# Kernel tuning notes

Measured on AMD Instinct MI355X. Metric: run time of the kernel, lower is better.

## Reference

```python
import jax, jax.numpy as jnp
import numpy as np

THETA = 10000.0
H, D_NOPE, D_ROPE, D_V = 12, 64, 64, 128
D_MODEL, D_LAT = 768, 128
B, S = 4, 2048


def _rope(x, pos, theta=THETA):
    # x: (B, S, D) with D even; pos: (S,) int. Matches RoPE.forward exactly
    # (interleaved even/odd rotation, freqs over full flattened D).
    D = x.shape[-1]
    inv_freq = 1.0 / theta ** (jnp.arange(0, D, 2, dtype=jnp.float32) / D)
    ang = pos.astype(jnp.float32)[:, None] * inv_freq        # (S, D/2)
    c, s = jnp.cos(ang), jnp.sin(ang)
    xe, xo = x[..., 0::2], x[..., 1::2]
    out = jnp.stack([xe * c - xo * s, xe * s + xo * c], axis=-1)
    return out.reshape(x.shape)


def setup_inputs() -> dict:
    key = jax.random.key(0)
    ks = jax.random.split(key, 12)
    std = 0.02
    inp = {
        'x': jax.random.normal(ks[0], (B, S, D_MODEL), jnp.float32),
        'token_positions': jnp.arange(S, dtype=jnp.int64) if jax.config.jax_enable_x64 else jnp.arange(S, dtype=jnp.int32),
        'W_dkv': jax.random.normal(ks[1], (D_LAT, D_MODEL), jnp.float32) * std,
        'b_dkv': jnp.zeros((D_LAT,), jnp.float32),
        'W_dq': jax.random.normal(ks[2], (D_LAT, D_MODEL), jnp.float32) * std,
        'b_dq': jnp.zeros((D_LAT,), jnp.float32),
        'W_uk_nope': jax.random.normal(ks[3], (H * D_NOPE, D_LAT), jnp.float32) * std,
        'b_uk_nope': jnp.zeros((H * D_NOPE,), jnp.float32),
        'W_uv': jax.random.normal(ks[4], (H * D_V, D_LAT), jnp.float32) * std,
        'b_uv': jnp.zeros((H * D_V,), jnp.float32),
        'W_uq_nope': jax.random.normal(ks[5], (H * D_NOPE, D_LAT), jnp.float32) * std,
        'b_uq_nope': jnp.zeros((H * D_NOPE,), jnp.float32),
        'W_uq_rope': jax.random.normal(ks[6], (H * D_ROPE, D_LAT), jnp.float32) * std,
        'b_uq_rope': jnp.zeros((H * D_ROPE,), jnp.float32),
        'W_uk_rope': jax.random.normal(ks[7], (H * D_ROPE, D_MODEL), jnp.float32) * std,
        'b_uk_rope': jnp.zeros((H * D_ROPE,), jnp.float32),
        'W_o': jax.random.normal(ks[8], (D_MODEL, H * D_V), jnp.float32) * std,
        'b_o': jnp.zeros((D_MODEL,), jnp.float32),
    }
    return inp


def reference(x, token_positions, W_dkv, b_dkv, W_dq, b_dq,
              W_uk_nope, b_uk_nope, W_uv, b_uv, W_uq_nope, b_uq_nope,
              W_uq_rope, b_uq_rope, W_uk_rope, b_uk_rope, W_o, b_o):
    b, s, _ = x.shape
    lin = lambda t, W, bb: t @ W.T + bb
    d_qk = D_NOPE + D_ROPE  # 128

    C_kv = lin(x, W_dkv, b_dkv)               # (B,S,128)
    C_q = lin(x, W_dq, b_dq)                  # (B,S,128)

    q_nope = lin(C_q, W_uq_nope, b_uq_nope)   # (B,S,H*64)
    k_nope = lin(C_kv, W_uk_nope, b_uk_nope)  # (B,S,H*64)
    v = lin(C_kv, W_uv, b_uv)                 # (B,S,H*128)

    q_rope = _rope(lin(C_q, W_uq_rope, b_uq_rope), token_positions)
    k_rope = _rope(lin(x, W_uk_rope, b_uk_rope), token_positions)

    # Faithful to torch: concat flattened nope||rope then view into heads.
    q = jnp.concatenate([q_nope, q_rope], axis=-1).reshape(b, s, H, d_qk).transpose(0, 2, 1, 3)
    k = jnp.concatenate([k_nope, k_rope], axis=-1).reshape(b, s, H, d_qk).transpose(0, 2, 1, 3)
    vh = v.reshape(b, s, H, D_V).transpose(0, 2, 1, 3)

    scale = 1.0 / jnp.sqrt(jnp.asarray(d_qk, x.dtype))
    logits = jnp.einsum('bhqd,bhkd->bhqk', q, k) * scale
    causal = jnp.tril(jnp.ones((s, s), bool))
    logits = jnp.where(causal, logits, jnp.finfo(logits.dtype).min)
    attn = jax.nn.softmax(logits, axis=-1)
    o = jnp.einsum('bhqk,bhkd->bhqd', attn, vh)      # (B,H,S,Dv)
    o = o.transpose(0, 2, 1, 3).reshape(b, s, H * D_V)
    return o @ W_o.T + b_o
```

## Files before the change

### kernel.cpp

```cpp
#include <hip/hip_runtime.h>

typedef __attribute__((ext_vector_type(8))) short short8;
typedef __attribute__((ext_vector_type(4))) short short4v;
typedef __attribute__((ext_vector_type(2))) int int2v;
typedef __attribute__((ext_vector_type(4))) float float4v;

#define MFMA16(a, b, c) __builtin_amdgcn_mfma_f32_16x16x32_bf16((a), (b), (c), 0, 0, 0)

__device__ __forceinline__ short f2bf(float f) {
  unsigned u = __float_as_uint(f);
  u += 0x7fffu + ((u >> 16) & 1u);
  return (short)(u >> 16);
}

__device__ __forceinline__ int cvtpk(float a, float b) {
  int r;
  asm("v_cvt_pk_bf16_f32 %0, %1, %2" : "=v"(r) : "v"(a), "v"(b));
  return r;
}

__device__ __forceinline__ void glds16(const short* g, short* l) {
  __builtin_amdgcn_global_load_lds(
      (const __attribute__((address_space(1))) void*)g,
      (__attribute__((address_space(3))) void*)l, 16, 0, 0);
}

struct CastSeg { const float* src; short* dst; int n4; };
struct CastArgs { CastSeg seg[9]; int start[10]; };

__global__ __launch_bounds__(256) void castk(CastArgs a) {
  int blk = blockIdx.x;
  int si = 0;
#pragma unroll
  for (int i = 1; i < 9; i++) si += (blk >= a.start[i]);
  int i = (blk - a.start[si]) * 256 + threadIdx.x;
  if (i >= a.seg[si].n4) return;
  float4v f = ((const float4v*)a.seg[si].src)[i];
  short4v o;
  o[0] = f2bf(f[0]); o[1] = f2bf(f[1]); o[2] = f2bf(f[2]); o[3] = f2bf(f[3]);
  ((short4v*)a.seg[si].dst)[i] = o;
}

struct GSeg {
  const short* A;
  const short* W;
  const float* bias0;
  const float* bias1;
  void* outp;
  int lda, ldw, bsplit, ropestart, ldo, ocol, K, flags;
};
struct GArgs { GSeg s[3]; int start[4]; };

__device__ __forceinline__ void gemm_body(const GArgs& ga, const int* __restrict__ pos) {
  int by = blockIdx.y;
  int si = (by >= ga.start[1]) + (by >= ga.start[2]);
  const GSeg sg = ga.s[si];
  int tid = threadIdx.x, w = tid >> 6, lane = tid & 63;
  int quad = lane >> 4, l16 = lane & 15;
  bool ropeF = sg.flags & 1, scaleF = sg.flags & 2;
  bool vtF = sg.flags & 4, f32F = sg.flags & 8, pairF = sg.flags & 16;
  int bm = blockIdx.x * 128;
  int bn = (by - ga.start[si]) * (pairF ? 256 : 128);
  int wm = (w & 1) * 64, wn = (w >> 1) * 64;
  int lda = sg.lda, ldw = sg.ldw;

  __shared__ short At[2][128 * 64];
  __shared__ short Bt[2][128 * 64];

  int srow[4], soff[4];
#pragma unroll
  for (int j = 0; j < 4; j++) {
    int r = w * 32 + j * 8 + (lane >> 3);
    srow[j] = r;
    soff[j] = ((lane & 7) ^ (r & 7)) << 3;
  }
  const short* Ag = sg.A + (size_t)bm * lda;
  const short* Wg = sg.W + (size_t)bn * ldw;

  float4v acc[4][4];
  float4v z = {0.f, 0.f, 0.f, 0.f};
#pragma unroll
  for (int mi = 0; mi < 4; mi++)
#pragma unroll
    for (int ni = 0; ni < 4; ni++) acc[mi][ni] = z;

  auto comp = [&](const short* Ab, const short* Bb) {
#pragma unroll
    for (int ks = 0; ks < 2; ks++) {
      short8 af[4], bf[4];
#pragma unroll
      for (int mi = 0; mi < 4; mi++) {
        int row = wm + mi * 16 + l16;
        af[mi] = *(const short8*)&Ab[(row << 6) + ((((ks << 2) + quad) ^ (row & 7)) << 3)];
      }
#pragma unroll
      for (int ni = 0; ni < 4; ni++) {
        int row = wn + ni * 16 + l16;
        bf[ni] = *(const short8*)&Bb[(row << 6) + ((((ks << 2) + quad) ^ (row & 7)) << 3)];
      }
#pragma unroll
      for (int mi = 0; mi < 4; mi++)
#pragma unroll
        for (int ni = 0; ni < 4; ni++)
          acc[mi][ni] = MFMA16(af[mi], bf[ni], acc[mi][ni]);
    }
  };

  auto epi = [&](int bnX) {
    if (vtF) {
      __syncthreads();
      short* T = &At[0][0];
#pragma unroll
      for (int ni = 0; ni < 4; ni++) {
        int col = wn + ni * 16 + l16;
        float bv = sg.bias0[bnX + col];
#pragma unroll
        for (int mi = 0; mi < 4; mi++) {
          int row0 = wm + mi * 16 + quad * 4;
          int rr = (row0 + ((col & 15) << 3)) & 127;
          short4v ov;
#pragma unroll
          for (int r = 0; r < 4; r++) ov[r] = f2bf(acc[mi][ni][r] + bv);
          *(short4v*)&T[col * 128 + rr] = ov;
        }
      }
      __syncthreads();
      int bidx = bm >> 11, s0 = bm & 2047;
      int sc = tid & 15;
#pragma unroll
      for (int cc = 0; cc < 8; cc++) {
        int c = cc * 16 + (tid >> 4);
        int rr = ((sc + (c & 15)) << 3) & 127;
        short8 v = *(const short8*)&T[c * 128 + rr];
        *(short8*)((short*)sg.outp + ((size_t)(bidx * 1536 + bnX + c)) * 2048 +
                   s0 + (sc << 3)) = v;
      }
      return;
    }
#pragma unroll
    for (int ni = 0; ni < 4; ni++) {
      int col = bnX + wn + ni * 16 + l16;
      float bv = (col < sg.bsplit) ? sg.bias0[col] : sg.bias1[col - sg.bsplit];
      float fr = 0.f;
      bool dorope = ropeF && (col >= sg.ropestart);
      if (dorope) {
        int ri = (col - sg.ropestart) & ~1;
        fr = exp2f((float)ri * (-13.287712379549449f / 768.0f));
      }
#pragma unroll
      for (int mi = 0; mi < 4; mi++) {
        int row0 = bm + wm + mi * 16 + quad * 4;
#pragma unroll
        for (int r = 0; r < 4; r++) {
          int row = row0 + r;
          float v = acc[mi][ni][r] + bv;
          if (ropeF) {
            float pv = __shfl_xor(v, 1, 64);
            if (dorope) {
              float ang = (float)pos[row & 2047] * fr;
              float sn, cs;
              __sincosf(ang, &sn, &cs);
              v = (col & 1) ? (pv * sn + v * cs) : (v * cs - pv * sn);
            }
          }
          if (scaleF) v *= 0.12751743f;
          if (f32F)
            ((float*)sg.outp)[(size_t)row * sg.ldo + sg.ocol + col] = v;
          else
            ((short*)sg.outp)[(size_t)row * sg.ldo + sg.ocol + col] = f2bf(v);
        }
      }
    }
  };

  int nk = sg.K >> 6;
  if (nk == 2) {
    auto stageB = [&](const short* Wg2) {
#pragma unroll
      for (int j = 0; j < 4; j++) {
        glds16(Wg2 + (size_t)srow[j] * ldw + soff[j], &Bt[0][(w * 32 + j * 8) * 64]);
        glds16(Wg2 + (size_t)srow[j] * ldw + 64 + soff[j], &Bt[1][(w * 32 + j * 8) * 64]);
      }
    };
#pragma unroll
    for (int j = 0; j < 4; j++) {
      glds16(Ag + (size_t)srow[j] * lda + soff[j], &At[0][(w * 32 + j * 8) * 64]);
      glds16(Ag + (size_t)srow[j] * lda + 64 + soff[j], &At[1][(w * 32 + j * 8) * 64]);
    }
    stageB(Wg);
    __syncthreads();
    comp(At[0], Bt[0]);
    comp(At[1], Bt[1]);
    if (pairF) {
      __syncthreads();
      stageB(Wg + (size_t)128 * ldw);
      epi(bn);
#pragma unroll
      for (int mi = 0; mi < 4; mi++)
#pragma unroll
        for (int ni = 0; ni < 4; ni++) acc[mi][ni] = z;
      __syncthreads();
      comp(At[0], Bt[0]);
      comp(At[1], Bt[1]);
      epi(bn + 128);
    } else {
      epi(bn);
    }
  } else {
#pragma unroll
    for (int j = 0; j < 4; j++)
      glds16(Ag + (size_t)srow[j] * lda + soff[j], &At[0][(w * 32 + j * 8) * 64]);
#pragma unroll
    for (int j = 0; j < 4; j++)
      glds16(Wg + (size_t)srow[j] * ldw + soff[j], &Bt[0][(w * 32 + j * 8) * 64]);
    for (int it = 0; it < nk; it++) {
      __syncthreads();
      if (it + 1 < nk) {
        int kt = (it + 1) << 6, nb = (it + 1) & 1;
#pragma unroll
        for (int j = 0; j < 4; j++)
          glds16(Ag + (size_t)srow[j] * lda + kt + soff[j],
                 &At[nb][(w * 32 + j * 8) * 64]);
#pragma unroll
        for (int j = 0; j < 4; j++)
          glds16(Wg + (size_t)srow[j] * ldw + kt + soff[j],
                 &Bt[nb][(w * 32 + j * 8) * 64]);
      }
      comp(At[it & 1], Bt[it & 1]);
    }
    epi(bn);
  }
}

__global__ __launch_bounds__(256, 2) void gemm_c(GArgs ga, const int* __restrict__ pos) {
  gemm_body(ga, pos);
}
__global__ __launch_bounds__(256, 2) void gemm_q(GArgs ga, const int* __restrict__ pos) {
  gemm_body(ga, pos);
}
__global__ __launch_bounds__(256, 2) void gemm_o(GArgs ga, const int* __restrict__ pos) {
  gemm_body(ga, pos);
}

__global__ __launch_bounds__(256, 2) void mla_attn(const short* __restrict__ Q,
                                                   const short* __restrict__ K,
                                                   const short* __restrict__ Vt,
                                                   short* __restrict__ O) {
  const int ld = 1536, SEQ = 2048;
  int tid = threadIdx.x, w = tid >> 6, lane = tid & 63;
  int quad = lane >> 4, l16 = lane & 15;
  int o = (int)blockIdx.x;
  int rank = o / 48;
  int g = o - rank * 48;
  int qt = (15 - rank) * 128;
  int hh = g % 12, b = g / 12;
  int qw = qt + w * 32;

  __shared__ short Kt[2][64 * 128];
  __shared__ short Vl[2][128 * 64];
  __shared__ short Pm[4][32 * 64];
  char* pwB = (char*)Pm[w];

  int kgo[4], vgo[4];
#pragma unroll
  for (int j = 0; j < 4; j++) {
    int rk = (w * 4 + j) * 4 + (lane >> 4);
    kgo[j] = rk * ld + (((lane & 15) ^ (rk & 7)) << 3);
    int rv = (w * 4 + j) * 8 + (lane >> 3);
    vgo[j] = rv * SEQ + (((lane & 7) ^ (rv & 7)) << 3);
  }
  const short* Kg = K + (size_t)b * SEQ * ld + hh * 128;
  const short* Vg = Vt + (size_t)(b * 12 + hh) * 128 * SEQ;

  short8 qf[2][4];
  {
    const short* Qg = Q + (size_t)(b * SEQ + qw + l16) * ld + hh * 128 + quad * 8;
#pragma unroll
    for (int nf = 0; nf < 2; nf++)
#pragma unroll
      for (int ks = 0; ks < 4; ks++)
        qf[nf][ks] = *(const short8*)(Qg + (size_t)nf * 16 * ld + ks * 32);
  }

  int koff[4][4], voff[2][8], pfo[2][2], pwo[2][4];
#pragma unroll
  for (int ks = 0; ks < 4; ks++)
#pragma unroll
    for (int mf = 0; mf < 4; mf++) {
      int row = mf * 16 + l16;
      koff[ks][mf] = row * 256 + ((((ks << 2) + quad) ^ (row & 7)) << 4);
    }
#pragma unroll
  for (int t = 0; t < 2; t++) {
#pragma unroll
    for (int df = 0; df < 8; df++) {
      int vr = df * 16 + l16;
      voff[t][df] = vr * 128 + ((((t << 2) + quad) ^ (vr & 7)) << 4);
    }
#pragma unroll
    for (int mq = 0; mq < 2; mq++)
      pfo[t][mq] = (mq * 16 + l16) * 128 + ((((t << 2) + quad) ^ (l16 & 7)) << 4);
#pragma unroll
    for (int mf = 0; mf < 4; mf++) {
      int p = (mf * 2 + (quad >> 1)) ^ (l16 & 7);
      pwo[t][mf] = (t * 16 + l16) * 128 + (p << 4) + ((quad & 1) << 3);
    }
  }

  float4v z = {0.f, 0.f, 0.f, 0.f};
  float4v oacc[2][8];
#pragma unroll
  for (int mq = 0; mq < 2; mq++)
#pragma unroll
    for (int df = 0; df < 8; df++) oacc[mq][df] = z;
  float l_i[2] = {0.f, 0.f};

#pragma unroll
  for (int j = 0; j < 4; j++) glds16(Kg + kgo[j], &Kt[0][(w * 4 + j) * 512]);
#pragma unroll
  for (int j = 0; j < 4; j++) glds16(Vg + vgo[j], &Vl[0][(w * 4 + j) * 512]);

  int ntiles = (qt >> 6) + 2;

#define ATTN_TILE(IT, NB, NB1)                                                 \
  do {                                                                         \
    int kt = (IT) << 6;                                                        \
    __syncthreads();                                                           \
    if ((IT) + 1 < ntiles) {                                                   \
      const short* kn = Kg + (size_t)(kt + 64) * ld;                           \
      const short* vn = Vg + (kt + 64);                                        \
      _Pragma("unroll") for (int j = 0; j < 4; j++)                            \
          glds16(kn + kgo[j], &Kt[NB1][(w * 4 + j) * 512]);                    \
      _Pragma("unroll") for (int j = 0; j < 4; j++)                            \
          glds16(vn + vgo[j], &Vl[NB1][(w * 4 + j) * 512]);                    \
    }                                                                          \
    if (kt <= qw + 31) {                                                       \
      const char* Kb = (const char*)Kt[NB];                                    \
      const char* Vb = (const char*)Vl[NB];                                    \
      float4v sf[4][2];                                                        \
      __builtin_amdgcn_s_setprio(1);                                           \
      _Pragma("unroll") for (int mf = 0; mf < 4; mf++) {                       \
        short8 a = *(const short8*)(Kb + koff[0][mf]);                         \
        sf[mf][0] = MFMA16(a, qf[0][0], z);                                    \
        sf[mf][1] = MFMA16(a, qf[1][0], z);                                    \
      }                                                                        \
      _Pragma("unroll") for (int ks = 1; ks < 4; ks++) {                       \
        _Pragma("unroll") for (int mf = 0; mf < 4; mf++) {                     \
          short8 a = *(const short8*)(Kb + koff[ks][mf]);                      \
          sf[mf][0] = MFMA16(a, qf[0][ks], sf[mf][0]);                         \
          sf[mf][1] = MFMA16(a, qf[1][ks], sf[mf][1]);                         \
        }                                                                      \
      }                                                                        \
      __builtin_amdgcn_s_setprio(0);                                           \
      if (kt + 63 > qw) {                                                      \
        _Pragma("unroll") for (int mf = 0; mf < 4; mf++) {                     \
          int key = kt + mf * 16 + quad * 4;                                   \
          _Pragma("unroll") for (int nf = 0; nf < 2; nf++) {                   \
            int q = qw + nf * 16 + l16;                                        \
            _Pragma("unroll") for (int r = 0; r < 4; r++)                      \
                if (key + r > q) sf[mf][nf][r] = -3e38f;                       \
          }                                                                    \
        }                                                                      \
      }                                                                        \
      _Pragma("unroll") for (int nf = 0; nf < 2; nf++) {                       \
        float ps = 0.f;                                                        \
        _Pragma("unroll") for (int mf = 0; mf < 4; mf++)                       \
            _Pragma("unroll") for (int r = 0; r < 4; r++) {                    \
          float e = exp2f(sf[mf][nf][r]);                                      \
          sf[mf][nf][r] = e;                                                   \
          ps += e;                                                             \
        }                                                                      \
        l_i[nf] += ps;                                                         \
        _Pragma("unroll") for (int mf = 0; mf < 4; mf++) {                     \
          int2v pk;                                                            \
          pk[0] = cvtpk(sf[mf][nf][0], sf[mf][nf][1]);                         \
          pk[1] = cvtpk(sf[mf][nf][2], sf[mf][nf][3]);                         \
          *(int2v*)(pwB + pwo[nf][mf]) = pk;                                   \
        }                                                                      \
      }                                                                        \
      __builtin_amdgcn_s_setprio(1);                                           \
      _Pragma("unroll") for (int t = 0; t < 2; t++) {                          \
        short8 pf0 = *(const short8*)(pwB + pfo[t][0]);                        \
        short8 pf1 = *(const short8*)(pwB + pfo[t][1]);                        \
        _Pragma("unroll") for (int df = 0; df < 8; df++) {                     \
          short8 vf = *(const short8*)(Vb + voff[t][df]);                      \
          oacc[0][df] = MFMA16(pf0, vf, oacc[0][df]);                          \
          oacc[1][df] = MFMA16(pf1, vf, oacc[1][df]);                          \
        }                                                                      \
      }                                                                        \
      __builtin_amdgcn_s_setprio(0);                                           \
    }                                                                          \
  } while (0)

  for (int it = 0; it < ntiles; it += 2) {
    ATTN_TILE(it, 0, 1);
    ATTN_TILE(it + 1, 1, 0);
  }
#undef ATTN_TILE

  short* Og = O + (size_t)(b * SEQ + qw) * ld + hh * 128;
#pragma unroll
  for (int mq = 0; mq < 2; mq++) {
    float l = l_i[mq];
    l += __shfl_xor(l, 16, 64);
    l += __shfl_xor(l, 32, 64);
    float linv = 1.0f / l;
    float lb[4];
#pragma unroll
    for (int r = 0; r < 4; r++) lb[r] = __shfl(linv, (quad << 2) + r, 64);
#pragma unroll
    for (int df = 0; df < 8; df++)
#pragma unroll
      for (int r = 0; r < 4; r++)
        Og[(size_t)(mq * 16 + (quad << 2) + r) * ld + df * 16 + l16] =
            f2bf(oacc[mq][df][r] * lb[r]);
  }
}

extern "C" void kernel_launch(void* const* d_in, const int* in_sizes, int n_in,
                              void* d_out, int out_size, void* d_ws, size_t ws_size,
                              hipStream_t stream) {
  const int S = 2048, DM = 768, DL = 128, HD = 1536;
  const int M = 4 * S;
  const int BIG = 1 << 28;

  const float* x = (const float*)d_in[0];
  const int* pos = (const int*)d_in[1];
  const float* W_dkv = (const float*)d_in[2];
  const float* b_dkv = (const float*)d_in[3];
  const float* W_dq = (const float*)d_in[4];
  const float* b_dq = (const float*)d_in[5];
  const float* W_uk_nope = (const float*)d_in[6];
  const float* b_uk_nope = (const float*)d_in[7];
  const float* W_uv = (const float*)d_in[8];
  const float* b_uv = (const float*)d_in[9];
  const float* W_uq_nope = (const float*)d_in[10];
  const float* b_uq_nope = (const float*)d_in[11];
  const float* W_uq_rope = (const float*)d_in[12];
  const float* b_uq_rope = (const float*)d_in[13];
  const float* W_uk_rope = (const float*)d_in[14];
  const float* b_uk_rope = (const float*)d_in[15];
  const float* W_o = (const float*)d_in[16];
  const float* b_o = (const float*)d_in[17];

  char* p = (char*)d_ws;
  size_t off = 0;
  auto take = [&](size_t nelem) -> short* {
    short* r = (short*)(p + off);
    off += (nelem * 2 + 255) & ~(size_t)255;
    return r;
  };
  short* xb = take((size_t)M * DM);
  short* Wdq = take(DL * DM);
  short* Wdkv = take(DL * DM);
  short* Wuqnope = take(768 * DL);
  short* Wuqrope = take(768 * DL);
  short* Wuknope = take(768 * DL);
  short* Wuv = take(1536 * DL);
  short* Wukrope = take(768 * DM);
  short* Wo = take(768 * 1536);
  short* Cm = take((size_t)M * 256);
  short* Qm = take((size_t)M * HD);
  short* Km = take((size_t)M * HD);
  short* Vtm = take((size_t)M * HD);
  short* Om = take((size_t)M * HD);
  if (off > ws_size) return;

  CastArgs ca;
  const float* srcs[9] = {x, W_dq, W_dkv, W_uq_nope, W_uq_rope, W_uk_nope, W_uv, W_uk_rope, W_o};
  short* dsts[9] = {xb, Wdq, Wdkv, Wuqnope, Wuqrope, Wuknope, Wuv, Wukrope, Wo};
  int ns[9] = {M * DM, DL * DM, DL * DM, 768 * DL, 768 * DL, 768 * DL, 1536 * DL, 768 * DM, 768 * 1536};
  ca.start[0] = 0;
  for (int i = 0; i < 9; i++) {
    ca.seg[i].src = srcs[i];
    ca.seg[i].dst = dsts[i];
    ca.seg[i].n4 = ns[i] / 4;
    ca.start[i + 1] = ca.start[i] + (ca.seg[i].n4 + 255) / 256;
  }
  castk<<<dim3(ca.start[9]), dim3(256), 0, stream>>>(ca);

  GArgs g1;
  g1.s[0].A = xb;   g1.s[0].W = Wdq;      g1.s[0].bias0 = b_dq;      g1.s[0].bias1 = b_dkv;
  g1.s[0].outp = Cm; g1.s[0].lda = DM; g1.s[0].ldw = DM; g1.s[0].bsplit = 128;
  g1.s[0].ropestart = 0; g1.s[0].ldo = 256; g1.s[0].ocol = 0; g1.s[0].K = DM; g1.s[0].flags = 0;
  g1.s[1].A = xb;   g1.s[1].W = Wukrope;  g1.s[1].bias0 = b_uk_rope; g1.s[1].bias1 = b_uk_rope;
  g1.s[1].outp = Km; g1.s[1].lda = DM; g1.s[1].ldw = DM; g1.s[1].bsplit = BIG;
  g1.s[1].ropestart = 0; g1.s[1].ldo = HD; g1.s[1].ocol = 768; g1.s[1].K = DM; g1.s[1].flags = 1;
  g1.s[2] = g1.s[1];
  g1.start[0] = 0; g1.start[1] = 2; g1.start[2] = 8; g1.start[3] = 8;
  gemm_c<<<dim3(M / 128, 8), dim3(256), 0, stream>>>(g1, pos);

  GArgs g2;
  g2.s[0].A = Cm;   g2.s[0].W = Wuqnope;  g2.s[0].bias0 = b_uq_nope; g2.s[0].bias1 = b_uq_rope;
  g2.s[0].outp = Qm; g2.s[0].lda = 256; g2.s[0].ldw = DL; g2.s[0].bsplit = 768;
  g2.s[0].ropestart = 768; g2.s[0].ldo = HD; g2.s[0].ocol = 0; g2.s[0].K = DL;
  g2.s[0].flags = 1 | 2 | 16;
  g2.s[1].A = Cm + 128; g2.s[1].W = Wuknope; g2.s[1].bias0 = b_uk_nope; g2.s[1].bias1 = b_uk_nope;
  g2.s[1].outp = Km; g2.s[1].lda = 256; g2.s[1].ldw = DL; g2.s[1].bsplit = BIG;
  g2.s[1].ropestart = 0; g2.s[1].ldo = HD; g2.s[1].ocol = 0; g2.s[1].K = DL;
  g2.s[1].flags = 16;
  g2.s[2].A = Cm + 128; g2.s[2].W = Wuv;   g2.s[2].bias0 = b_uv;      g2.s[2].bias1 = b_uv;
  g2.s[2].outp = Vtm; g2.s[2].lda = 256; g2.s[2].ldw = DL; g2.s[2].bsplit = BIG;
  g2.s[2].ropestart = 0; g2.s[2].ldo = 0; g2.s[2].ocol = 0; g2.s[2].K = DL;
  g2.s[2].flags = 4;
  g2.start[0] = 0; g2.start[1] = 6; g2.start[2] = 9; g2.start[3] = 21;
  gemm_q<<<dim3(M / 128, 21), dim3(256), 0, stream>>>(g2, pos);

  mla_attn<<<dim3(768), dim3(256), 0, stream>>>(Qm, Km, Vtm, Om);

  GArgs g3;
  g3.s[0].A = Om;   g3.s[0].W = Wo;       g3.s[0].bias0 = b_o;       g3.s[0].bias1 = b_o;
  g3.s[0].outp = d_out; g3.s[0].lda = HD; g3.s[0].ldw = HD; g3.s[0].bsplit = BIG;
  g3.s[0].ropestart = 0; g3.s[0].ldo = 768; g3.s[0].ocol = 0; g3.s[0].K = HD; g3.s[0].flags = 8;
  g3.s[1] = g3.s[0];
  g3.s[2] = g3.s[0];
  g3.start[0] = 0; g3.start[1] = 6; g3.start[2] = 6; g3.start[3] = 6;
  gemm_o<<<dim3(M / 128, 6), dim3(256), 0, stream>>>(g3, pos);
}
```

Baseline: 306.8 us.

## Specialize latent up-projection GEMM with resident A tile and 256-wide N per block

Result: faster. 295.5 us (-3.7%).

```diff
diff --git a/kernel.cpp b/kernel.cpp
--- a/kernel.cpp
+++ b/kernel.cpp
@@ -174,39 +174,7 @@
   };
 
   int nk = sg.K >> 6;
-  if (nk == 2) {
-    auto stageB = [&](const short* Wg2) {
-#pragma unroll
-      for (int j = 0; j < 4; j++) {
-        glds16(Wg2 + (size_t)srow[j] * ldw + soff[j], &Bt[0][(w * 32 + j * 8) * 64]);
-        glds16(Wg2 + (size_t)srow[j] * ldw + 64 + soff[j], &Bt[1][(w * 32 + j * 8) * 64]);
-      }
-    };
-#pragma unroll
-    for (int j = 0; j < 4; j++) {
-      glds16(Ag + (size_t)srow[j] * lda + soff[j], &At[0][(w * 32 + j * 8) * 64]);
-      glds16(Ag + (size_t)srow[j] * lda + 64 + soff[j], &At[1][(w * 32 + j * 8) * 64]);
-    }
-    stageB(Wg);
-    __syncthreads();
-    comp(At[0], Bt[0]);
-    comp(At[1], Bt[1]);
-    if (pairF) {
-      __syncthreads();
-      stageB(Wg + (size_t)128 * ldw);
-      epi(bn);
-#pragma unroll
-      for (int mi = 0; mi < 4; mi++)
-#pragma unroll
-        for (int ni = 0; ni < 4; ni++) acc[mi][ni] = z;
-      __syncthreads();
-      comp(At[0], Bt[0]);
-      comp(At[1], Bt[1]);
-      epi(bn + 128);
-    } else {
-      epi(bn);
-    }
-  } else {
+  {
 #pragma unroll
     for (int j = 0; j < 4; j++)
       glds16(Ag + (size_t)srow[j] * lda + soff[j], &At[0][(w * 32 + j * 8) * 64]);
@@ -235,11 +203,147 @@
 __global__ __launch_bounds__(256, 2) void gemm_c(GArgs ga, const int* __restrict__ pos) {
   gemm_body(ga, pos);
 }
-__global__ __launch_bounds__(256, 2) void gemm_q(GArgs ga, const int* __restrict__ pos) {
-  gemm_body(ga, pos);
-}
 __global__ __launch_bounds__(256, 2) void gemm_o(GArgs ga, const int* __restrict__ pos) {
   gemm_body(ga, pos);
+}
+
+__global__ __launch_bounds__(256, 2) void gemm_q(GArgs ga, const int* __restrict__ pos) {
+  int by = blockIdx.y;
+  int si = (by >= ga.start[1]) + (by >= ga.start[2]);
+  const GSeg sg = ga.s[si];
+  int tid = threadIdx.x, w = tid >> 6, lane = tid & 63;
+  int quad = lane >> 4, l16 = lane & 15;
+  bool ropeF = sg.flags & 1, scaleF = sg.flags & 2, vtF = sg.flags & 4;
+  int bm = blockIdx.x * 128;
+  int bnu = (by - ga.start[si]) * 256;
+  int wm = (w & 1) * 64, wn = (w >> 1) * 32;
+
+  __shared__ short At[128 * 128];
+  __shared__ short Bt[2][64 * 128];
+  __shared__ short Tt[64 * 128];
+
+  const short* Ag = sg.A + (size_t)bm * 256;
+#pragma unroll
+  for (int j = 0; j < 8; j++) {
+    int rk = w * 32 + j * 4 + (lane >> 4);
+    glds16(Ag + (size_t)rk * 256 + ((l16 ^ (rk & 7)) << 3),
+           &At[(w * 32 + j * 4) * 128]);
+  }
+  const short* Wg0 = sg.W + (size_t)bnu * 128;
+  auto stageB = [&](int sub, short* dst) {
+    const short* Wg = Wg0 + (size_t)(sub * 64) * 128;
+#pragma unroll
+    for (int j = 0; j < 4; j++) {
+      int rk = w * 16 + j * 4 + (lane >> 4);
+      glds16(Wg + (size_t)rk * 128 + ((l16 ^ (rk & 7)) << 3),
+             &dst[(w * 16 + j * 4) * 128]);
+    }
+  };
+
+  float4v acc[4][2];
+  float4v z = {0.f, 0.f, 0.f, 0.f};
+#pragma unroll
+  for (int mi = 0; mi < 4; mi++)
+#pragma unroll
+    for (int ni = 0; ni < 2; ni++) acc[mi][ni] = z;
+
+  auto comp = [&](const short* Bb) {
+#pragma unroll
+    for (int ks = 0; ks < 4; ks++) {
+      short8 af[4], bf[2];
+#pragma unroll
+      for (int mi = 0; mi < 4; mi++) {
+        int row = wm + mi * 16 + l16;
+        af[mi] = *(const short8*)&At[(row << 7) + (((ks * 4 + quad) ^ (row & 7)) << 3)];
+      }
+#pragma unroll
+      for (int ni = 0; ni < 2; ni++) {
+        int row = wn + ni * 16 + l16;
+        bf[ni] = *(const short8*)&Bb[(row << 7) + (((ks * 4 + quad) ^ (row & 7)) << 3)];
+      }
+#pragma unroll
+      for (int mi = 0; mi < 4; mi++)
+#pragma unroll
+        for (int ni = 0; ni < 2; ni++)
+          acc[mi][ni] = MFMA16(af[mi], bf[ni], acc[mi][ni]);
+    }
+  };
+
+  auto epi = [&](int bnX) {
+    if (vtF) {
+      __syncthreads();
+#pragma unroll
+      for (int ni = 0; ni < 2; ni++) {
+        int col = wn + ni * 16 + l16;
+        float bv = sg.bias0[bnX + col];
+#pragma unroll
+        for (int mi = 0; mi < 4; mi++) {
+          int row0 = wm + mi * 16 + quad * 4;
+          int rr = (row0 + ((col & 15) << 3)) & 127;
+          short4v ov;
+#pragma unroll
+          for (int r = 0; r < 4; r++) ov[r] = f2bf(acc[mi][ni][r] + bv);
+          *(short4v*)&Tt[col * 128 + rr] = ov;
+        }
+      }
+      __syncthreads();
+      int bidx = bm >> 11, s0 = bm & 2047;
+      int sc = tid & 15;
+#pragma unroll
+      for (int cc = 0; cc < 4; cc++) {
+        int c = cc * 16 + (tid >> 4);
+        int rr = ((sc + (c & 15)) << 3) & 127;
+        short8 v = *(const short8*)&Tt[c * 128 + rr];
+        *(short8*)((short*)sg.outp + ((size_t)(bidx * 1536 + bnX + c)) * 2048 +
+                   s0 + (sc << 3)) = v;
+      }
+      return;
+    }
+#pragma unroll
+    for (int ni = 0; ni < 2; ni++) {
+      int col = bnX + wn + ni * 16 + l16;
+      float bv = (col < sg.bsplit) ? sg.bias0[col] : sg.bias1[col - sg.bsplit];
+      float fr = 0.f;
+      bool dorope = ropeF && (col >= sg.ropestart);
+      if (dorope) {
+        int ri = (col - sg.ropestart) & ~1;
+        fr = exp2f((float)ri * (-13.287712379549449f / 768.0f));
+      }
+#pragma unroll
+      for (int mi = 0; mi < 4; mi++) {
+        int row0 = bm + wm + mi * 16 + quad * 4;
+#pragma unroll
+        for (int r = 0; r < 4; r++) {
+          int row = row0 + r;
+          float v = acc[mi][ni][r] + bv;
+          if (ropeF) {
+            float pv = __shfl_xor(v, 1, 64);
+            if (dorope) {
+              float ang = (float)pos[row & 2047] * fr;
+              float sn, cs;
+              __sincosf(ang, &sn, &cs);
+              v = (col & 1) ? (pv * sn + v * cs) : (v * cs - pv * sn);
+            }
+          }
+          if (scaleF) v *= 0.12751743f;
+          ((short*)sg.outp)[(size_t)row * sg.ldo + sg.ocol + col] = f2bf(v);
+        }
+      }
+    }
+  };
+
+  stageB(0, Bt[0]);
+  __syncthreads();
+  for (int t = 0; t < 4; t++) {
+    if (t) __syncthreads();
+    if (t + 1 < 4) stageB(t + 1, Bt[(t + 1) & 1]);
+    comp(Bt[t & 1]);
+    epi(bnu + t * 64);
+#pragma unroll
+    for (int mi = 0; mi < 4; mi++)
+#pragma unroll
+      for (int ni = 0; ni < 2; ni++) acc[mi][ni] = z;
+  }
 }
 
 __global__ __launch_bounds__(256, 2) void mla_attn(const short* __restrict__ Q,
@@ -494,17 +598,17 @@
   g2.s[0].A = Cm;   g2.s[0].W = Wuqnope;  g2.s[0].bias0 = b_uq_nope; g2.s[0].bias1 = b_uq_rope;
   g2.s[0].outp = Qm; g2.s[0].lda = 256; g2.s[0].ldw = DL; g2.s[0].bsplit = 768;
   g2.s[0].ropestart = 768; g2.s[0].ldo = HD; g2.s[0].ocol = 0; g2.s[0].K = DL;
-  g2.s[0].flags = 1 | 2 | 16;
+  g2.s[0].flags = 1 | 2;
   g2.s[1].A = Cm + 128; g2.s[1].W = Wuknope; g2.s[1].bias0 = b_uk_nope; g2.s[1].bias1 = b_uk_nope;
   g2.s[1].outp = Km; g2.s[1].lda = 256; g2.s[1].ldw = DL; g2.s[1].bsplit = BIG;
   g2.s[1].ropestart = 0; g2.s[1].ldo = HD; g2.s[1].ocol = 0; g2.s[1].K = DL;
-  g2.s[1].flags = 16;
+  g2.s[1].flags = 0;
   g2.s[2].A = Cm + 128; g2.s[2].W = Wuv;   g2.s[2].bias0 = b_uv;      g2.s[2].bias1 = b_uv;
   g2.s[2].outp = Vtm; g2.s[2].lda = 256; g2.s[2].ldw = DL; g2.s[2].bsplit = BIG;
   g2.s[2].ropestart = 0; g2.s[2].ldo = 0; g2.s[2].ocol = 0; g2.s[2].K = DL;
   g2.s[2].flags = 4;
-  g2.start[0] = 0; g2.start[1] = 6; g2.start[2] = 9; g2.start[3] = 21;
-  gemm_q<<<dim3(M / 128, 21), dim3(256), 0, stream>>>(g2, pos);
+  g2.start[0] = 0; g2.start[1] = 6; g2.start[2] = 9; g2.start[3] = 15;
+  gemm_q<<<dim3(M / 128, 15), dim3(256), 0, stream>>>(g2, pos);
 
   mla_attn<<<dim3(768), dim3(256), 0, stream>>>(Qm, Km, Vtm, Om);
 
```
